# Kernel tuning notes

Measured on AMD Instinct MI355X. Metric: run time of the kernel, lower is better.

The kernel has to match this reference:

```python
import jax, jax.numpy as jnp
import numpy as np

N, E, C, NB, NE, G = 20000, 320000, 64, 8, 4, 16
L2 = 9          # (max_ell+1)^2 with max_ell=2
RMAX = 5.0
HID = 16        # nonlinear readout hidden width


def setup_inputs():
    key = jax.random.key(0)
    ks = jax.random.split(key, 16)
    positions = jax.random.uniform(ks[0], (N, 3), dtype=jnp.float32) * 3.0
    elems = jax.random.randint(ks[1], (N,), 0, NE)
    node_attrs = jax.nn.one_hot(elems, NE, dtype=jnp.float32)
    edge_index = jax.random.randint(ks[2], (2, E), 0, N)
    batch = jnp.sort(jax.random.randint(ks[3], (N,), 0, G))
    shifts = jnp.zeros((E, 3), jnp.float32)
    atomic_energies = jnp.array([-1.0, -2.0, -3.0, -4.0], jnp.float32)
    sc = lambda k, shp, fan: jax.random.normal(k, shp, jnp.float32) / np.sqrt(fan).astype(np.float32)
    W_embed = sc(ks[4], (NE, C), NE)
    W_up = sc(ks[5], (2, C, C), C)
    W1 = sc(ks[6], (2, NB, 64), NB)
    W2 = sc(ks[7], (2, 64, C), 64)
    W_out = sc(ks[8], (2, C, C), C)
    W_skip = sc(ks[9], (2, NE, C), NE)
    w_read0 = sc(ks[10], (C,), C)
    W_r1 = sc(ks[11], (C, HID), C)
    w_r2 = sc(ks[12], (HID,), HID)
    return dict(positions=positions, node_attrs=node_attrs, shifts=shifts,
                atomic_energies=atomic_energies, W_embed=W_embed, W_up=W_up,
                W1=W1, W2=W2, W_out=W_out, W_skip=W_skip, w_read0=w_read0,
                W_r1=W_r1, w_r2=w_r2, edge_index=edge_index, batch=batch)


def _sph_harm_l2(u):
    # component-normalized real spherical harmonics up to l=2 on unit vectors
    x, y, z = u[:, 0], u[:, 1], u[:, 2]
    s3, s5, s15 = jnp.sqrt(3.0), jnp.sqrt(5.0), jnp.sqrt(15.0)
    return jnp.stack([jnp.ones_like(x),
                      s3 * x, s3 * y, s3 * z,
                      s15 * x * y, s15 * y * z, 0.5 * s5 * (3.0 * z * z - 1.0),
                      s15 * x * z, 0.5 * s15 * (x * x - y * y)], axis=-1)


def _radial(r):
    # Bessel radial basis with polynomial cutoff (p=6)
    n = jnp.arange(1, NB + 1, dtype=jnp.float32)
    rb = jnp.sqrt(2.0 / RMAX) * jnp.sin(n * jnp.pi * r[:, None] / RMAX) / r[:, None]
    u = r / RMAX
    fc = 1.0 - 28.0 * u**6 + 48.0 * u**7 - 21.0 * u**8
    fc = jnp.where(u < 1.0, fc, 0.0)
    return rb * fc[:, None]


def _energy_contributions(positions, node_attrs, shifts, atomic_energies,
                          W_embed, W_up, W1, W2, W_out, W_skip,
                          w_read0, W_r1, w_r2, edge_index, batch):
    snd, rcv = edge_index[0], edge_index[1]
    vec = positions[snd] - positions[rcv] + shifts                  # [E,3]
    r = jnp.sqrt(jnp.sum(vec * vec, axis=-1) + 1e-12)               # [E]
    Y = _sph_harm_l2(vec / r[:, None])                              # [E,L2]
    ef = _radial(r)                                                 # [E,NB]
    # E0: per-element reference energies, summed per graph
    e0 = jax.ops.segment_sum(node_attrs @ atomic_energies, batch, num_segments=G)
    h0 = node_attrs @ W_embed                                       # [N,C] scalar feats
    h = jnp.zeros((positions.shape[0], L2, C), h0.dtype).at[:, 0, :].set(h0)
    readouts = [lambda s: s @ w_read0,
                lambda s: jax.nn.silu(s @ W_r1) @ w_r2]             # linear / nonlinear
    energies = [e0]
    for i in range(2):
        hu = jnp.einsum('nlc,cd->nld', h, W_up[i])                  # channel mix
        R = jax.nn.silu(ef @ W1[i]) @ W2[i]                         # radial MLP [E,C]
        s = jnp.einsum('elc,el->ec', hu[snd], Y)                    # equivariant contraction
        m = Y[:, :, None] * (R * s)[:, None, :]                     # [E,L2,C] messages
        agg = jax.ops.segment_sum(m, rcv, num_segments=positions.shape[0])
        h = jnp.einsum('nlc,cd->nld', agg, W_out[i])
        h = h.at[:, 0, :].add(node_attrs @ W_skip[i])               # scalar skip connection
        node_en = readouts[i](h[:, 0, :])                           # [N]
        energies.append(jax.ops.segment_sum(node_en, batch, num_segments=G))
    return jnp.stack(energies, axis=-1)                             # [G, num_interactions+1]


def reference(positions, node_attrs, shifts, atomic_energies, W_embed, W_up,
              W1, W2, W_out, W_skip, w_read0, W_r1, w_r2, edge_index, batch):
    contributions = _energy_contributions(positions, node_attrs, shifts,
        atomic_energies, W_embed, W_up, W1, W2, W_out, W_skip,
        w_read0, W_r1, w_r2, edge_index, batch)
    total_energy = jnp.sum(contributions, axis=-1)                  # [G]
    forces = -jax.grad(lambda p: jnp.sum(_energy_contributions(p, node_attrs,
        shifts, atomic_energies, W_embed, W_up, W1, W2, W_out, W_skip,
        w_read0, W_r1, w_r2, edge_index, batch)))(positions)        # [N,3]
    return total_energy, contributions, forces
```

## Files before the change

kernel.cpp:

```cpp
#include <hip/hip_runtime.h>
#include <cmath>

constexpr int N_  = 20000;
constexpr int E_  = 320000;
constexpr int NE_ = 4;
constexpr int G_  = 16;
constexpr int CAP = 96;
constexpr int TAB = 4096;
constexpr float RMAXF = 5.0f;
constexpr float PI_F  = 3.14159265358979323846f;
constexpr float S3  = 1.7320508075688772f;
constexpr float S5  = 2.2360679774997896f;
constexpr float S15 = 3.8729833462074170f;
constexpr float KC_ = 0.6324555320336759f;

typedef unsigned short u16;
typedef unsigned int   u32;
typedef _Float16 f16;
typedef _Float16 f16x2 __attribute__((ext_vector_type(2)));

#define DEV static __device__ __forceinline__

__device__ float g_fallback[110000000];

DEV float sigmoidf_(float x){ return 1.0f/(1.0f+__expf(-x)); }

DEV float b2f(u16 u){ return __uint_as_float(((u32)u)<<16); }
DEV u16  f2b(float f){
  u32 x = __float_as_uint(f);
  return (u16)((x + 0x7FFFu + ((x>>16)&1u)) >> 16);
}
DEV u16  f2h(float f){ union{f16 h; u16 u;} v; v.h=(f16)f; return v.u; }
DEV float h2f(u16 u){ union{u16 u2; f16 h;} v; v.u2=u; return (float)v.h; }

DEV f16x2 u2h(u32 x){ union{u32 u; f16x2 h;} v; v.u=x; return v.h; }
DEV u32 h2u(f16x2 h){ union{u32 u; f16x2 h;} v; v.h=h; return v.u; }
DEV u32 pkh(float a, float b){ f16x2 h; h.x=(f16)a; h.y=(f16)b; return h2u(h); }

DEV void ld4(const float* __restrict__ p, float* d){
  float4 a = ((const float4*)p)[0];
  d[0]=a.x; d[1]=a.y; d[2]=a.z; d[3]=a.w;
}
DEV void st8h(u16* p, const float* d){
  uint4 v;
  v.x = pkh(d[0],d[1]); v.y = pkh(d[2],d[3]);
  v.z = pkh(d[4],d[5]); v.w = pkh(d[6],d[7]);
  *(uint4*)p = v;
}
DEV void ldY(const u16* __restrict__ p, float* Yb){
  ushort4 a = *(const ushort4*)p;
  ushort4 b = *(const ushort4*)(p+4);
  Yb[0]=h2f(a.x); Yb[1]=h2f(a.y); Yb[2]=h2f(a.z); Yb[3]=h2f(a.w);
  Yb[4]=h2f(b.x); Yb[5]=h2f(b.y); Yb[6]=h2f(b.z); Yb[7]=h2f(b.w);
}

DEV float tlerp(const u16* __restrict__ tab, int i0, float f, int idx){
  return h2f(tab[i0*256+idx])*(1.0f-f) + h2f(tab[(i0+1)*256+idx])*f;
}

__global__ void k_cnt(const int* __restrict__ ei, int* __restrict__ cntR){
  int e = blockIdx.x*256 + threadIdx.x;
  atomicAdd(&cntR[ei[E_+e]], 1);
}

__global__ void k_scan(const int* __restrict__ cntR, int* __restrict__ offR){
  __shared__ int part[256];
  int t = threadIdx.x;
  constexpr int CH = (N_+255)/256;
  int base = t*CH;
  int s=0;
  for (int i=0;i<CH;++i){ int idx=base+i; if(idx<N_) s+=cntR[idx]; }
  part[t]=s; __syncthreads();
  for (int d=1; d<256; d<<=1){
    int v = (t>=d)? part[t-d] : 0;
    __syncthreads();
    part[t]+=v;
    __syncthreads();
  }
  int run = (t==0)?0:part[t-1];
  for (int i=0;i<CH;++i){ int idx=base+i; if(idx<N_){ offR[idx]=run; run+=cntR[idx]; } }
  if (t==255) offR[N_]=run;
}

__global__ void k_perm(const int* __restrict__ ei, const int* __restrict__ offR,
                       int* __restrict__ cntR2, int* __restrict__ cntS,
                       int* __restrict__ pe, int* __restrict__ pSnd, int* __restrict__ pRcv,
                       int* __restrict__ listS){
  int e = blockIdx.x*256 + threadIdx.x;
  int s = ei[e], r = ei[E_+e];
  int p = offR[r] + atomicAdd(&cntR2[r], 1);
  pe[p] = e; pSnd[p] = s; pRcv[p] = r;
  int q = atomicAdd(&cntS[s], 1); if (q < CAP) listS[s*CAP+q] = p;
}

__global__ void k_pre(const float* __restrict__ Wout0, const float* __restrict__ Wup1,
                      const float* __restrict__ Wskip0, const float* __restrict__ wread0,
                      const float* __restrict__ Wemb, const float* __restrict__ Wup0,
                      const float* __restrict__ Wr1, const float* __restrict__ Wout1,
                      float* __restrict__ WA, float* __restrict__ sa,
                      float* __restrict__ va, float* __restrict__ sv,
                      float* __restrict__ WembUp, float* __restrict__ CC){
  int t = threadIdx.x;
  for (int idx=t; idx<4096; idx+=256){
    int c = idx>>6, d = idx&63;
    float acc=0.f;
    for (int m=0;m<64;++m) acc += Wout0[c*64+m]*Wup1[m*64+d];
    WA[idx]=acc;
  }
  {
    int k = t>>6, d = t&63;
    float acc=0.f;
    for (int m=0;m<64;++m) acc += Wskip0[k*64+m]*Wup1[m*64+d];
    sa[t]=acc;
    float acc2=0.f;
    for (int j=0;j<64;++j) acc2 += Wemb[k*64+j]*Wup0[j*64+d];
    WembUp[t]=acc2;
  }
  for (int idx=t; idx<1024; idx+=256){
    int j = idx>>6, c = idx&63;
    float acc=0.f;
    for (int k=0;k<64;++k) acc += Wr1[k*16+j]*Wout1[c*64+k];
    CC[idx]=acc;
  }
  if (t<64){
    float acc=0.f;
    for (int d=0;d<64;++d) acc += Wout0[t*64+d]*wread0[d];
    va[t]=acc;
  }
  if (t<4){
    float acc=0.f;
    for (int d=0;d<64;++d) acc += Wskip0[t*64+d]*wread0[d];
    sv[t]=acc;
  }
}

__global__ __launch_bounds__(256, 2)
void k_rtab(const float* __restrict__ W1g, const float* __restrict__ W2g,
            u16* __restrict__ tab){
  __shared__ float sW1[1024];
  __shared__ u32   sW2h[4096];
  __shared__ u32   sAh[32*36];
  int t = threadIdx.x;
  for (int i=t;i<1024;i+=256) sW1[i]=W1g[i];
  for (int i=t;i<4096;i+=256){
    int L = i>>11, rem = i&2047, kp = rem>>6, c = rem&63;
    sW2h[i] = pkh(W2g[L*4096 + (2*kp)*64 + c], W2g[L*4096 + (2*kp+1)*64 + c]);
  }
  __syncthreads();
  int wid=t>>6, lane=t&63, q=lane>>3, j=lane&7, c0=j*8;
  int slot = wid*8 + q;
  int knot = blockIdx.x*32 + slot;
  bool valid = (knot <= TAB);
  float rad = fmaxf((float)knot * (RMAXF/(float)TAB), 1e-6f);
  float inv = 1.0f/rad;
  float tt = rad*(1.0f/RMAXF);
  float fc = 0.0f, dfc = 0.0f;
  if (tt < 1.0f){
    float t2=tt*tt, t4=t2*t2, t5=t4*tt, t6=t5*tt, t7=t6*tt, t8=t7*tt;
    fc  = 1.0f - 28.0f*t6 + 48.0f*t7 - 21.0f*t8;
    dfc = (-168.0f*t5 + 336.0f*t6 - 168.0f*t7)*(1.0f/RMAXF);
  }
  float th = rad*(PI_F/RMAXF);
  float s1 = __sinf(th), c1 = __cosf(th);
  float base = KC_*inv*fc;
  float efv[8], gfv[8];
  {
    float sb = s1, cb = c1;
    #pragma unroll
    for (int b=0;b<8;++b){
      efv[b] = base*sb;
      float wb_ = (float)(b+1)*(PI_F/RMAXF);
      float rb  = KC_*sb*inv;
      float drb = KC_*(wb_*cb - sb*inv)*inv;
      gfv[b] = drb*fc + rb*dfc;
      float sn = sb*c1 + cb*s1;
      cb = cb*c1 - sb*s1;
      sb = sn;
    }
  }
  u32* myAh = sAh + slot*36;
  for (int L=0; L<2; ++L){
    const float* w1 = sW1 + L*512;
    const u32*  w2h = sW2h + L*2048;
    float zz[8]={0,0,0,0,0,0,0,0};
    float wgv[8]={0,0,0,0,0,0,0,0};
    #pragma unroll 4
    for (int b=0;b<8;++b){
      float efb = efv[b], gfb = gfv[b];
      const float4* w=(const float4*)(w1 + b*64 + c0);
      float4 wa=w[0], wb=w[1];
      zz[0]+=efb*wa.x; zz[1]+=efb*wa.y; zz[2]+=efb*wa.z; zz[3]+=efb*wa.w;
      zz[4]+=efb*wb.x; zz[5]+=efb*wb.y; zz[6]+=efb*wb.z; zz[7]+=efb*wb.w;
      wgv[0]+=gfb*wa.x; wgv[1]+=gfb*wa.y; wgv[2]+=gfb*wa.z; wgv[3]+=gfb*wa.w;
      wgv[4]+=gfb*wb.x; wgv[5]+=gfb*wb.y; wgv[6]+=gfb*wb.z; wgv[7]+=gfb*wb.w;
    }
    float a[8], dv[8];
    #pragma unroll
    for (int i=0;i<8;++i){
      float sg = sigmoidf_(zz[i]);
      a[i]  = zz[i]*sg;
      float sp = sg*(1.0f + zz[i]*(1.0f - sg));
      dv[i] = wgv[i]*sp;
    }
    {
      uint4 av;
      av.x = pkh(a[0],a[1]); av.y = pkh(a[2],a[3]);
      av.z = pkh(a[4],a[5]); av.w = pkh(a[6],a[7]);
      *(uint4*)(myAh + 4*j) = av;
    }
    {
      float r0=0.f,r1=0.f,r2=0.f,r3=0.f,r4=0.f,r5=0.f,r6=0.f,r7=0.f;
      #pragma unroll 2
      for (int kp4=0; kp4<8; ++kp4){
        uint4 dq = *(const uint4*)(myAh + 4*kp4);
        #pragma unroll
        for (int i=0;i<4;++i){
          u32 du = (i==0)?dq.x:(i==1)?dq.y:(i==2)?dq.z:dq.w;
          f16x2 dh = u2h(du);
          const u32* wrow = w2h + (4*kp4+i)*64 + c0;
          uint4 w0 = *(const uint4*)(wrow);
          uint4 w1v = *(const uint4*)(wrow+4);
          r0 = __builtin_amdgcn_fdot2(dh, u2h(w0.x),  r0, false);
          r1 = __builtin_amdgcn_fdot2(dh, u2h(w0.y),  r1, false);
          r2 = __builtin_amdgcn_fdot2(dh, u2h(w0.z),  r2, false);
          r3 = __builtin_amdgcn_fdot2(dh, u2h(w0.w),  r3, false);
          r4 = __builtin_amdgcn_fdot2(dh, u2h(w1v.x), r4, false);
          r5 = __builtin_amdgcn_fdot2(dh, u2h(w1v.y), r5, false);
          r6 = __builtin_amdgcn_fdot2(dh, u2h(w1v.z), r6, false);
          r7 = __builtin_amdgcn_fdot2(dh, u2h(w1v.w), r7, false);
        }
      }
      float racc[8] = {r0,r1,r2,r3,r4,r5,r6,r7};
      if (valid) st8h(tab + (size_t)knot*256 + L*64 + c0, racc);
    }
    {
      uint4 av;
      av.x = pkh(dv[0],dv[1]); av.y = pkh(dv[2],dv[3]);
      av.z = pkh(dv[4],dv[5]); av.w = pkh(dv[6],dv[7]);
      *(uint4*)(myAh + 4*j) = av;
    }
    {
      float r0=0.f,r1=0.f,r2=0.f,r3=0.f,r4=0.f,r5=0.f,r6=0.f,r7=0.f;
      #pragma unroll 2
      for (int kp4=0; kp4<8; ++kp4){
        uint4 dq = *(const uint4*)(myAh + 4*kp4);
        #pragma unroll
        for (int i=0;i<4;++i){
          u32 du = (i==0)?dq.x:(i==1)?dq.y:(i==2)?dq.z:dq.w;
          f16x2 dh = u2h(du);
          const u32* wrow = w2h + (4*kp4+i)*64 + c0;
          uint4 w0 = *(const uint4*)(wrow);
          uint4 w1v = *(const uint4*)(wrow+4);
          r0 = __builtin_amdgcn_fdot2(dh, u2h(w0.x),  r0, false);
          r1 = __builtin_amdgcn_fdot2(dh, u2h(w0.y),  r1, false);
          r2 = __builtin_amdgcn_fdot2(dh, u2h(w0.z),  r2, false);
          r3 = __builtin_amdgcn_fdot2(dh, u2h(w0.w),  r3, false);
          r4 = __builtin_amdgcn_fdot2(dh, u2h(w1v.x), r4, false);
          r5 = __builtin_amdgcn_fdot2(dh, u2h(w1v.y), r5, false);
          r6 = __builtin_amdgcn_fdot2(dh, u2h(w1v.z), r6, false);
          r7 = __builtin_amdgcn_fdot2(dh, u2h(w1v.w), r7, false);
        }
      }
      float qacc[8] = {r0,r1,r2,r3,r4,r5,r6,r7};
      if (valid) st8h(tab + (size_t)knot*256 + 128 + L*64 + c0, qacc);
    }
  }
}

__global__ void k_fwd_edge(const float* __restrict__ pos, const float* __restrict__ shifts,
                const int* __restrict__ pe, const int* __restrict__ pSnd,
                const int* __restrict__ pRcv,
                u16* __restrict__ Y, float* __restrict__ u3,
                float* __restrict__ irr, float* __restrict__ xi){
  int e = blockIdx.x*256 + threadIdx.x;
  int eo  = pe[e];
  int snd = pSnd[e], rcv = pRcv[e];
  float vx = pos[snd*3+0]-pos[rcv*3+0]+shifts[(size_t)eo*3+0];
  float vy = pos[snd*3+1]-pos[rcv*3+1]+shifts[(size_t)eo*3+1];
  float vz = pos[snd*3+2]-pos[rcv*3+2]+shifts[(size_t)eo*3+2];
  float ss = vx*vx+vy*vy+vz*vz + 1e-12f;
  float rad = sqrtf(ss);
  float inv = 1.0f/rad;
  float x = vx*inv, y = vy*inv, z = vz*inv;
  irr[e]=inv;
  xi[e] = rad * ((float)TAB/RMAXF);
  u3[(size_t)e*3+0]=x; u3[(size_t)e*3+1]=y; u3[(size_t)e*3+2]=z;
  float Yf[8];
  Yf[0]=S3*x; Yf[1]=S3*y; Yf[2]=S3*z;
  Yf[3]=S15*x*y; Yf[4]=S15*y*z;
  Yf[5]=0.5f*S5*(3.0f*z*z-1.0f);
  Yf[6]=S15*x*z;
  Yf[7]=0.5f*S15*(x*x-y*y);
  st8h(Y + (size_t)e*8, Yf);
}

__global__ void k_agg0(const int* __restrict__ offR, const int* __restrict__ pSnd,
                       const float* __restrict__ attrs, const float* __restrict__ WembUp,
                       const u16* __restrict__ tab, const float* __restrict__ xi,
                       const u16* __restrict__ Y,
                       u16* __restrict__ agg0){
  int t = threadIdx.x; int n = blockIdx.x*4 + (t>>6); int c = t&63;
  float we0 = WembUp[0*64+c], we1 = WembUp[1*64+c], we2 = WembUp[2*64+c], we3 = WembUp[3*64+c];
  float acc[9] = {0,0,0,0,0,0,0,0,0};
  int p0 = offR[n], p1 = offR[n+1];
  for (int p=p0;p<p1;++p){
    int s = pSnd[p];
    float xiv = xi[p];
    float r0v = 0.f;
    if (xiv < (float)TAB){
      int i0 = (int)xiv; float f = xiv - (float)i0;
      r0v = tlerp(tab, i0, f, c);
    }
    float4 av = *(const float4*)(attrs + (size_t)s*4);
    float hu0c = av.x*we0 + av.y*we1 + av.z*we2 + av.w*we3;
    float v = r0v*hu0c;
    float Yb[8];
    ldY(Y + (size_t)p*8, Yb);
    acc[0] += v;
    #pragma unroll
    for (int l=1;l<9;++l) acc[l] += Yb[l-1]*v;
  }
  #pragma unroll
  for (int l=0;l<9;++l) agg0[((size_t)n*9+l)*64+c] = f2h(acc[l]);
}

__global__ void k_s1(const int* __restrict__ cntS, const int* __restrict__ listS,
                     const u16* __restrict__ hu1, const u16* __restrict__ Y,
                     u16* __restrict__ s1){
  int t = threadIdx.x; int n = blockIdx.x*4 + (t>>6); int c = t&63;
  float hu[9];
  #pragma unroll
  for (int l=0;l<9;++l) hu[l] = b2f(hu1[((size_t)n*9+l)*64+c]);
  int deg = min(cntS[n], CAP);
  #pragma unroll 2
  for (int j=0;j<deg;++j){
    int p = listS[n*CAP+j];
    float Yb[8];
    ldY(Y + (size_t)p*8, Yb);
    float acc = hu[0];
    #pragma unroll
    for (int l=1;l<9;++l) acc += hu[l]*Yb[l-1];
    s1[(size_t)p*64+c] = f2h(acc);
  }
}

__global__ void k_agg1(const int* __restrict__ offR,
                       const u16* __restrict__ tab, const float* __restrict__ xi,
                       const u16* __restrict__ s1,
                       float* __restrict__ agg1){
  int t = threadIdx.x; int n = blockIdx.x*4 + (t>>6); int c = t&63;
  float acc = 0.f;
  int p0 = offR[n], p1 = offR[n+1];
  for (int p=p0;p<p1;++p){
    float xiv = xi[p];
    float r1v = 0.f;
    if (xiv < (float)TAB){
      int i0 = (int)xiv; float f = xiv - (float)i0;
      r1v = tlerp(tab, i0, f, 64 + c);
    }
    acc += r1v*h2f(s1[(size_t)p*64+c]);
  }
  agg1[(size_t)n*64+c] = acc;
}

__global__ void k_dhu1(const int* __restrict__ cntS, const int* __restrict__ listS,
                       const int* __restrict__ pRcv,
                       const u16* __restrict__ tab, const float* __restrict__ xi,
                       const float* __restrict__ ga1, const u16* __restrict__ Y,
                       u16* __restrict__ dhu1){
  int t = threadIdx.x; int n = blockIdx.x*4 + (t>>6); int c = t&63;
  float acc[9] = {0,0,0,0,0,0,0,0,0};
  int deg = min(cntS[n], CAP);
  #pragma unroll 2
  for (int j=0;j<deg;++j){
    int p = listS[n*CAP+j];
    int r = pRcv[p];
    float xiv = xi[p];
    float r1v = 0.f;
    if (xiv < (float)TAB){
      int i0 = (int)xiv; float f = xiv - (float)i0;
      r1v = tlerp(tab, i0, f, 64 + c);
    }
    float ds = r1v*ga1[(size_t)r*64+c];
    float Yb[8];
    ldY(Y + (size_t)p*8, Yb);
    acc[0] += ds;
    #pragma unroll
    for (int l=1;l<9;++l) acc[l] += Yb[l-1]*ds;
  }
  #pragma unroll
  for (int l=0;l<9;++l) dhu1[((size_t)n*9+l)*64+c] = f2h(acc[l]);
}

template<bool TRANS, bool OUTB, bool IN16>
__global__ __launch_bounds__(256, 2)
void k_mm64(const void* __restrict__ in, const float* __restrict__ W,
            void* __restrict__ out, int rows, int lper,
            const float* __restrict__ attrs, const float* __restrict__ Wsk,
            const float* __restrict__ bias){
  __shared__ float sWT[64*68];
  __shared__ float sRow[4*68];
  int t = threadIdx.x;
  for (int i=t;i<4096;i+=256){
    int k=i&63, c=i>>6;
    sWT[c*68+k] = TRANS ? W[c*64+k] : W[k*64+c];
  }
  __syncthreads();
  int wid = t>>6, c = t&63;
  float wcol[64];
  {
    const float4* wp = (const float4*)(sWT + c*68);
    #pragma unroll
    for (int kk=0;kk<16;++kk){
      float4 w4 = wp[kk];
      wcol[4*kk+0]=w4.x; wcol[4*kk+1]=w4.y; wcol[4*kk+2]=w4.z; wcol[4*kk+3]=w4.w;
    }
  }
  float* myRow = sRow + wid*68;
  for (int it=0; it<8; ++it){
    int row = (blockIdx.x*8+it)*4 + wid;
    if (IN16) myRow[c] = h2f(((const u16*)in)[(size_t)row*64+c]);
    else      myRow[c] = ((const float*)in)[(size_t)row*64+c];
    float acc = 0.f;
    #pragma unroll
    for (int kk=0;kk<16;++kk){
      float4 r4 = ((const float4*)myRow)[kk];
      acc += r4.x*wcol[4*kk+0] + r4.y*wcol[4*kk+1] + r4.z*wcol[4*kk+2] + r4.w*wcol[4*kk+3];
    }
    if (lper==1 || (row % 9)==0){
      int n = (lper==1) ? row : (row/9);
      if (attrs){
        #pragma unroll
        for (int k=0;k<NE_;++k) acc += attrs[n*NE_+k]*Wsk[k*64+c];
      }
      if (bias) acc += bias[c];
    }
    if (OUTB) ((u16*)out)[(size_t)row*64+c] = f2b(acc);
    else      ((float*)out)[(size_t)row*64+c] = acc;
  }
}

__global__ void k_read0(const u16* __restrict__ agg0, const float* __restrict__ va,
                        const float* __restrict__ sv, const float* __restrict__ attrs,
                        const float* __restrict__ ae,
                        const int* __restrict__ batch, float* __restrict__ out){
  __shared__ float bins0[G_];
  __shared__ float bins1[G_];
  int t = threadIdx.x;
  if (t < G_){ bins0[t] = 0.f; bins1[t] = 0.f; }
  __syncthreads();
  int lane = t & 63, wid = t >> 6;
  int grp = lane >> 3, j = lane & 7;
  int n = blockIdx.x*32 + wid*8 + grp;
  const u16* hp = agg0 + (size_t)n*576 + j*8;
  float h[8];
  ldY(hp, h);
  const float* wp = va + j*8;
  float4 w0v = ((const float4*)wp)[0], w4v = ((const float4*)wp)[1];
  float v = h[0]*w0v.x + h[1]*w0v.y + h[2]*w0v.z + h[3]*w0v.w
          + h[4]*w4v.x + h[5]*w4v.y + h[6]*w4v.z + h[7]*w4v.w;
  v += __shfl_xor(v,1,64); v += __shfl_xor(v,2,64); v += __shfl_xor(v,4,64);
  if (j==0){
    float4 av = *(const float4*)(attrs + (size_t)n*4);
    v += av.x*sv[0] + av.y*sv[1] + av.z*sv[2] + av.w*sv[3];
    float e0v = av.x*ae[0] + av.y*ae[1] + av.z*ae[2] + av.w*ae[3];
    int b = batch[n];
    atomicAdd(&bins1[b], v);
    atomicAdd(&bins0[b], e0v);
  }
  __syncthreads();
  if (t < G_){
    float b0 = bins0[t], b1 = bins1[t];
    if (b0 != 0.f || b1 != 0.f){
      atomicAdd(&out[t], b0 + b1);
      if (b0 != 0.f) atomicAdd(&out[G_ + t*3 + 0], b0);
      if (b1 != 0.f) atomicAdd(&out[G_ + t*3 + 1], b1);
    }
  }
}

__global__ void k_read1(const float* __restrict__ h2, const float* __restrict__ Wr1,
                        const float* __restrict__ wr2, const int* __restrict__ batch,
                        const float* __restrict__ CC,
                        float* __restrict__ ga1, float* __restrict__ out){
  __shared__ float sW[64*16];
  __shared__ float sCC[16*64];
  __shared__ float sSp[256];
  __shared__ float sA[256];
  __shared__ float bins[G_];
  int t = threadIdx.x;
  for (int i=t;i<1024;i+=256){ sW[i]=Wr1[i]; sCC[i]=CC[i]; }
  if (t < G_) bins[t] = 0.f;
  __syncthreads();
  int nn = t>>4; int j = t&15;
  int n = blockIdx.x*16 + nn;
  float z = 0.f;
  #pragma unroll 16
  for (int c=0;c<64;++c) z += h2[(size_t)n*64+c]*sW[c*16+j];
  float sg = sigmoidf_(z);
  float a  = z*sg;
  float sp = sg*(1.0f + z*(1.0f - sg));
  float w2v = wr2[j];
  sSp[t] = sp*w2v;
  sA[t]  = a*w2v;
  __syncthreads();
  {
    int cb = j*4;
    float g0=0.f,g1=0.f,g2=0.f,g3=0.f;
    const float* sp_ = sSp + nn*16;
    #pragma unroll
    for (int jp=0;jp<16;++jp){
      float s = sp_[jp];
      const float* cc = sCC + jp*64 + cb;
      g0 += s*cc[0]; g1 += s*cc[1]; g2 += s*cc[2]; g3 += s*cc[3];
    }
    *(float4*)(ga1 + (size_t)n*64 + cb) = make_float4(g0,g1,g2,g3);
  }
  if (j==0){
    float s = 0.f;
    #pragma unroll
    for (int k=0;k<16;++k) s += sA[nn*16+k];
    atomicAdd(&bins[batch[n]], s);
  }
  __syncthreads();
  if (t < G_){
    float b = bins[t];
    if (b != 0.f){
      atomicAdd(&out[t], b);
      atomicAdd(&out[G_ + t*3 + 2], b);
    }
  }
}

__global__ __launch_bounds__(256, 4)
void k_bedge_all(const int* __restrict__ pSnd, const int* __restrict__ pRcv,
             const u16* __restrict__ Y,
             const float* __restrict__ u3, const float* __restrict__ irr,
             const u16* __restrict__ tab, const float* __restrict__ xi,
             const float* __restrict__ ga1, const u16* __restrict__ ga0,
             const float* __restrict__ attrs, const float* __restrict__ WembUp,
             const u16* __restrict__ hu1,
             float* __restrict__ gF){
  int t = threadIdx.x;
  int wid=t>>6, lane=t&63, q=lane>>4, j=lane&15, c0=j*4;
  int slot = wid*4+q;
  int e = blockIdx.x*16 + slot;
  int snd = pSnd[e], rcv = pRcv[e];
  float wembr[4][4];
  #pragma unroll
  for (int k=0;k<4;++k){
    float4 wr = *(const float4*)(WembUp + k*64 + c0);
    wembr[k][0]=wr.x; wembr[k][1]=wr.y; wembr[k][2]=wr.z; wembr[k][3]=wr.w;
  }
  float Yl[9];
  Yl[0]=1.0f;
  ldY(Y + (size_t)e*8, Yl+1);
  ushort4 huv1[9];
  #pragma unroll
  for (int l=0;l<9;++l) huv1[l] = *(const ushort4*)(hu1 + ((size_t)snd*9 + l)*64 + c0);
  ushort4 gv0[9];
  #pragma unroll
  for (int l=0;l<9;++l) gv0[l] = *(const ushort4*)(ga0 + ((size_t)rcv*9 + l)*64 + c0);
  float T1[4];  ld4(ga1 + (size_t)rcv*64 + c0, T1);
  float4 av = *(const float4*)(attrs + (size_t)snd*4);
  float hu0v[4];
  #pragma unroll
  for (int i=0;i<4;++i)
    hu0v[i] = av.x*wembr[0][i] + av.y*wembr[1][i] + av.z*wembr[2][i] + av.w*wembr[3][i];
  float xiv = xi[e];
  float R0v[4], R1v[4], q0v[4], q1v[4];
  if (xiv < (float)TAB){
    int i0 = (int)xiv; float f = xiv - (float)i0, g = 1.0f - f;
    const u16* ra = tab + (size_t)i0*256;
    const u16* rb = ra + 256;
    ushort4 a, b;
    a = *(const ushort4*)(ra + c0);        b = *(const ushort4*)(rb + c0);
    R0v[0]=h2f(a.x)*g+h2f(b.x)*f; R0v[1]=h2f(a.y)*g+h2f(b.y)*f;
    R0v[2]=h2f(a.z)*g+h2f(b.z)*f; R0v[3]=h2f(a.w)*g+h2f(b.w)*f;
    a = *(const ushort4*)(ra + 64 + c0);   b = *(const ushort4*)(rb + 64 + c0);
    R1v[0]=h2f(a.x)*g+h2f(b.x)*f; R1v[1]=h2f(a.y)*g+h2f(b.y)*f;
    R1v[2]=h2f(a.z)*g+h2f(b.z)*f; R1v[3]=h2f(a.w)*g+h2f(b.w)*f;
    a = *(const ushort4*)(ra + 128 + c0);  b = *(const ushort4*)(rb + 128 + c0);
    q0v[0]=h2f(a.x)*g+h2f(b.x)*f; q0v[1]=h2f(a.y)*g+h2f(b.y)*f;
    q0v[2]=h2f(a.z)*g+h2f(b.z)*f; q0v[3]=h2f(a.w)*g+h2f(b.w)*f;
    a = *(const ushort4*)(ra + 192 + c0);  b = *(const ushort4*)(rb + 192 + c0);
    q1v[0]=h2f(a.x)*g+h2f(b.x)*f; q1v[1]=h2f(a.y)*g+h2f(b.y)*f;
    q1v[2]=h2f(a.z)*g+h2f(b.z)*f; q1v[3]=h2f(a.w)*g+h2f(b.w)*f;
  } else {
    #pragma unroll
    for (int i=0;i<4;++i){ R0v[i]=0.f; R1v[i]=0.f; q0v[i]=0.f; q1v[i]=0.f; }
  }
  float dyp[9];
  float dR1[4];
  {
    float ds1[4], sA[4];
    #pragma unroll
    for (int i=0;i<4;++i){ ds1[i]=R1v[i]*T1[i]; sA[i]=0.f; }
    #pragma unroll
    for (int l=0;l<9;++l){
      float h0v=b2f(huv1[l].x), h1v=b2f(huv1[l].y), h2v=b2f(huv1[l].z), h3v=b2f(huv1[l].w);
      float Ylv = Yl[l];
      sA[0]+=h0v*Ylv; sA[1]+=h1v*Ylv; sA[2]+=h2v*Ylv; sA[3]+=h3v*Ylv;
      dyp[l] = ds1[0]*h0v + ds1[1]*h1v + ds1[2]*h2v + ds1[3]*h3v;
    }
    #pragma unroll
    for (int i=0;i<4;++i) dR1[i]=sA[i]*T1[i];
  }
  float dR0[4];
  {
    float P[4], T0[4];
    #pragma unroll
    for (int i=0;i<4;++i){ P[i]=R0v[i]*hu0v[i]; T0[i]=0.f; }
    #pragma unroll
    for (int l=0;l<9;++l){
      float g0=b2f(gv0[l].x), g1=b2f(gv0[l].y), g2=b2f(gv0[l].z), g3=b2f(gv0[l].w);
      float Ylv = Yl[l];
      T0[0]+=g0*Ylv; T0[1]+=g1*Ylv; T0[2]+=g2*Ylv; T0[3]+=g3*Ylv;
      dyp[l] += g0*P[0] + g1*P[1] + g2*P[2] + g3*P[3];
    }
    #pragma unroll
    for (int i=0;i<4;++i) dR0[i]=hu0v[i]*T0[i];
  }
  float dy[9];
  #pragma unroll
  for (int l=1;l<9;++l){
    float v=dyp[l];
    v += __shfl_xor(v,1,64); v += __shfl_xor(v,2,64);
    v += __shfl_xor(v,4,64); v += __shfl_xor(v,8,64);
    dy[l]=v;
  }
  float dr = q1v[0]*dR1[0]+q1v[1]*dR1[1]+q1v[2]*dR1[2]+q1v[3]*dR1[3]
           + q0v[0]*dR0[0]+q0v[1]*dR0[1]+q0v[2]*dR0[2]+q0v[3]*dR0[3];
  dr += __shfl_xor(dr,1,64); dr += __shfl_xor(dr,2,64);
  dr += __shfl_xor(dr,4,64); dr += __shfl_xor(dr,8,64);
  float x = u3[(size_t)e*3+0], y = u3[(size_t)e*3+1], zz = u3[(size_t)e*3+2];
  float invr = irr[e];
  float dux = S3*dy[1] + S15*(y*dy[4] + zz*dy[7] + x*dy[8]);
  float duy = S3*dy[2] + S15*(x*dy[4] + zz*dy[5] - y*dy[8]);
  float duz = S3*dy[3] + S15*(y*dy[5] + x*dy[7]) + 3.0f*S5*zz*dy[6];
  float udot = x*dux + y*duy + zz*duz;
  float gx = dr*x + invr*(dux - x*udot);
  float gy = dr*y + invr*(duy - y*udot);
  float gz = dr*zz + invr*(duz - zz*udot);
  if (j==0){
    float* gp2 = gF + (size_t)e*3;
    gp2[0]=gx; gp2[1]=gy; gp2[2]=gz;
  }
}

__global__ void k_fsum(const int* __restrict__ offR, const int* __restrict__ cntS,
                       const int* __restrict__ listS,
                       const float* __restrict__ gF, float* __restrict__ F){
  int t = threadIdx.x;
  int lane = t & 63, wid = t >> 6;
  int sub = lane >> 3, j = lane & 7;
  int n = blockIdx.x*32 + wid*8 + sub;
  float fx=0.f, fy=0.f, fz=0.f;
  int p0 = offR[n], p1 = offR[n+1];
  for (int p=p0+j; p<p1; p+=8){
    fx += gF[(size_t)p*3+0]; fy += gF[(size_t)p*3+1]; fz += gF[(size_t)p*3+2];
  }
  int dSn = min(cntS[n], CAP);
  for (int k=j;k<dSn;k+=8){
    int p = listS[n*CAP+k];
    fx -= gF[(size_t)p*3+0]; fy -= gF[(size_t)p*3+1]; fz -= gF[(size_t)p*3+2];
  }
  fx += __shfl_xor(fx,1,64); fy += __shfl_xor(fy,1,64); fz += __shfl_xor(fz,1,64);
  fx += __shfl_xor(fx,2,64); fy += __shfl_xor(fy,2,64); fz += __shfl_xor(fz,2,64);
  fx += __shfl_xor(fx,4,64); fy += __shfl_xor(fy,4,64); fz += __shfl_xor(fz,4,64);
  if (j==0){
    F[n*3+0]=fx; F[n*3+1]=fy; F[n*3+2]=fz;
  }
}

extern "C" void kernel_launch(void* const* d_in, const int* in_sizes, int n_in,
                              void* d_out, int out_size, void* d_ws, size_t ws_size,
                              hipStream_t stream){
  (void)in_sizes; (void)n_in;
  const float* pos    = (const float*)d_in[0];
  const float* attrs  = (const float*)d_in[1];
  const float* shifts = (const float*)d_in[2];
  const float* ae     = (const float*)d_in[3];
  const float* Wemb   = (const float*)d_in[4];
  const float* Wup    = (const float*)d_in[5];
  const float* W1     = (const float*)d_in[6];
  const float* W2     = (const float*)d_in[7];
  const float* Wout   = (const float*)d_in[8];
  const float* Wskip  = (const float*)d_in[9];
  const float* wread0 = (const float*)d_in[10];
  const float* Wr1    = (const float*)d_in[11];
  const float* wr2    = (const float*)d_in[12];
  const int*   ei     = (const int*)d_in[13];
  const int*   batch  = (const int*)d_in[14];
  float* out = (float*)d_out;

  const size_t NEED = 430000000;
  char* base;
  if (ws_size >= NEED){
    base = (char*)d_ws;
  } else {
    void* p = nullptr;
    hipGetSymbolAddress(&p, HIP_SYMBOL(g_fallback));
    base = (char*)p;
  }
  size_t off = 0;
  auto alloc = [&](size_t bytes)->char*{
    char* p = base + off;
    off += ((bytes + 255)/256)*256;
    return p;
  };
  u16*   Y    = (u16*)  alloc((size_t)E_*8*2);
  float* u3   = (float*)alloc((size_t)E_*3*4);
  float* irr  = (float*)alloc((size_t)E_*4);
  float* xi   = (float*)alloc((size_t)E_*4);
  u16*   s1b  = (u16*)  alloc((size_t)E_*64*2);
  float* gF   = (float*)alloc((size_t)E_*3*4);
  u16*   tab  = (u16*)  alloc((size_t)(TAB+1)*256*2);
  u16*   hu1  = (u16*)  alloc((size_t)N_*9*64*2);
  u16*   agg0 = (u16*)  alloc((size_t)N_*9*64*2);
  float* agg1 = (float*)alloc((size_t)N_*64*4);
  float* h2   = (float*)alloc((size_t)N_*64*4);
  float* ga1  = (float*)alloc((size_t)N_*64*4);
  u16*   ga0  = (u16*)  alloc((size_t)N_*9*64*2);
  float* WembUp = (float*)alloc(256*4);
  float* WA   = (float*)alloc(4096*4);
  float* sa   = (float*)alloc(256*4);
  float* va   = (float*)alloc(64*4);
  float* sv   = (float*)alloc(4*4);
  float* CC   = (float*)alloc(1024*4);
  int* cnts  = (int*)alloc((size_t)3*N_*4);
  int* offR  = (int*)alloc((size_t)(N_+1)*4);
  int* pe    = (int*)alloc((size_t)E_*4);
  int* pSnd  = (int*)alloc((size_t)E_*4);
  int* pRcv  = (int*)alloc((size_t)E_*4);
  int* listS = (int*)alloc((size_t)N_*CAP*4);
  int* cntR = cnts;  int* cntS = cnts + N_;  int* cntR2 = cnts + 2*N_;
  u16* dhu1 = agg0;
  float* F = out + G_ + G_*3;

  hipMemsetAsync(d_out, 0, (size_t)out_size*sizeof(float), stream);
  hipMemsetAsync(cnts, 0, (size_t)3*N_*sizeof(int), stream);

  k_cnt     <<<E_/256, 256, 0, stream>>>(ei, cntR);
  k_scan    <<<1, 256, 0, stream>>>(cntR, offR);
  k_perm    <<<E_/256, 256, 0, stream>>>(ei, offR, cntR2, cntS, pe, pSnd, pRcv, listS);

  k_rtab    <<<(TAB+1+31)/32, 256, 0, stream>>>(W1, W2, tab);
  k_fwd_edge<<<E_/256, 256, 0, stream>>>(pos, shifts, pe, pSnd, pRcv, Y, u3, irr, xi);
  k_pre     <<<1, 256, 0, stream>>>(Wout, Wup + 4096, Wskip, wread0, Wemb, Wup, Wr1, Wout + 4096, WA, sa, va, sv, WembUp, CC);
  k_agg0    <<<N_/4, 256, 0, stream>>>(offR, pSnd, attrs, WembUp, tab, xi, Y, agg0);
  k_mm64<false,true,true><<<N_*9/32, 256, 0, stream>>>(agg0, WA, hu1, N_*9, 9, attrs, sa, nullptr);
  k_read0   <<<N_/32, 256, 0, stream>>>(agg0, va, sv, attrs, ae, batch, out);
  k_s1      <<<N_/4, 256, 0, stream>>>(cntS, listS, hu1, Y, s1b);
  k_agg1    <<<N_/4, 256, 0, stream>>>(offR, tab, xi, s1b, agg1);
  k_mm64<false,false,false><<<N_/32, 256, 0, stream>>>(agg1, Wout + 4096, h2, N_, 1, attrs, Wskip + 256, nullptr);
  k_read1   <<<N_/16, 256, 0, stream>>>(h2, Wr1, wr2, batch, CC, ga1, out);

  k_dhu1    <<<N_/4, 256, 0, stream>>>(cntS, listS, pRcv, tab, xi, ga1, Y, dhu1);
  k_mm64<true,true,true><<<N_*9/32, 256, 0, stream>>>(dhu1, WA, ga0, N_*9, 9, nullptr, nullptr, va);
  k_bedge_all<<<E_/16, 256, 0, stream>>>(pSnd, pRcv, Y, u3, irr, tab, xi, ga1, ga0, attrs, WembUp, hu1, gF);
  k_fsum    <<<N_/32, 256, 0, stream>>>(offR, cntS, listS, gF, F);
}
```

Before: 727.6 us.

## Split per-node edge loops across two wavefronts and defer loads in backward edge kernel

```diff
diff --git a/kernel.cpp b/kernel.cpp
--- a/kernel.cpp
+++ b/kernel.cpp
@@ -299,11 +299,14 @@
                        const u16* __restrict__ tab, const float* __restrict__ xi,
                        const u16* __restrict__ Y,
                        u16* __restrict__ agg0){
-  int t = threadIdx.x; int n = blockIdx.x*4 + (t>>6); int c = t&63;
+  __shared__ float red[2][9][64];
+  int t = threadIdx.x; int wid = t>>6; int c = t&63;
+  int nl = wid>>1, half = wid&1;
+  int n = blockIdx.x*2 + nl;
   float we0 = WembUp[0*64+c], we1 = WembUp[1*64+c], we2 = WembUp[2*64+c], we3 = WembUp[3*64+c];
   float acc[9] = {0,0,0,0,0,0,0,0,0};
   int p0 = offR[n], p1 = offR[n+1];
-  for (int p=p0;p<p1;++p){
+  for (int p=p0+half; p<p1; p+=2){
     int s = pSnd[p];
     float xiv = xi[p];
     float r0v = 0.f;
@@ -320,20 +323,28 @@
     #pragma unroll
     for (int l=1;l<9;++l) acc[l] += Yb[l-1]*v;
   }
-  #pragma unroll
-  for (int l=0;l<9;++l) agg0[((size_t)n*9+l)*64+c] = f2h(acc[l]);
+  if (half==1){
+    #pragma unroll
+    for (int l=0;l<9;++l) red[nl][l][c] = acc[l];
+  }
+  __syncthreads();
+  if (half==0){
+    #pragma unroll
+    for (int l=0;l<9;++l) agg0[((size_t)n*9+l)*64+c] = f2h(acc[l] + red[nl][l][c]);
+  }
 }
 
 __global__ void k_s1(const int* __restrict__ cntS, const int* __restrict__ listS,
                      const u16* __restrict__ hu1, const u16* __restrict__ Y,
                      u16* __restrict__ s1){
-  int t = threadIdx.x; int n = blockIdx.x*4 + (t>>6); int c = t&63;
+  int t = threadIdx.x; int wid = t>>6; int c = t&63;
+  int nl = wid>>1, half = wid&1;
+  int n = blockIdx.x*2 + nl;
   float hu[9];
   #pragma unroll
   for (int l=0;l<9;++l) hu[l] = b2f(hu1[((size_t)n*9+l)*64+c]);
   int deg = min(cntS[n], CAP);
-  #pragma unroll 2
-  for (int j=0;j<deg;++j){
+  for (int j=half;j<deg;j+=2){
     int p = listS[n*CAP+j];
     float Yb[8];
     ldY(Y + (size_t)p*8, Yb);
@@ -348,10 +359,13 @@
                        const u16* __restrict__ tab, const float* __restrict__ xi,
                        const u16* __restrict__ s1,
                        float* __restrict__ agg1){
-  int t = threadIdx.x; int n = blockIdx.x*4 + (t>>6); int c = t&63;
+  __shared__ float red[2][64];
+  int t = threadIdx.x; int wid = t>>6; int c = t&63;
+  int nl = wid>>1, half = wid&1;
+  int n = blockIdx.x*2 + nl;
   float acc = 0.f;
   int p0 = offR[n], p1 = offR[n+1];
-  for (int p=p0;p<p1;++p){
+  for (int p=p0+half; p<p1; p+=2){
     float xiv = xi[p];
     float r1v = 0.f;
     if (xiv < (float)TAB){
@@ -360,7 +374,9 @@
     }
     acc += r1v*h2f(s1[(size_t)p*64+c]);
   }
-  agg1[(size_t)n*64+c] = acc;
+  if (half==1) red[nl][c] = acc;
+  __syncthreads();
+  if (half==0) agg1[(size_t)n*64+c] = acc + red[nl][c];
 }
 
 __global__ void k_dhu1(const int* __restrict__ cntS, const int* __restrict__ listS,
@@ -368,11 +384,13 @@
                        const u16* __restrict__ tab, const float* __restrict__ xi,
                        const float* __restrict__ ga1, const u16* __restrict__ Y,
                        u16* __restrict__ dhu1){
-  int t = threadIdx.x; int n = blockIdx.x*4 + (t>>6); int c = t&63;
+  __shared__ float red[2][9][64];
+  int t = threadIdx.x; int wid = t>>6; int c = t&63;
+  int nl = wid>>1, half = wid&1;
+  int n = blockIdx.x*2 + nl;
   float acc[9] = {0,0,0,0,0,0,0,0,0};
   int deg = min(cntS[n], CAP);
-  #pragma unroll 2
-  for (int j=0;j<deg;++j){
+  for (int j=half;j<deg;j+=2){
     int p = listS[n*CAP+j];
     int r = pRcv[p];
     float xiv = xi[p];
@@ -388,8 +406,15 @@
     #pragma unroll
     for (int l=1;l<9;++l) acc[l] += Yb[l-1]*ds;
   }
-  #pragma unroll
-  for (int l=0;l<9;++l) dhu1[((size_t)n*9+l)*64+c] = f2h(acc[l]);
+  if (half==1){
+    #pragma unroll
+    for (int l=0;l<9;++l) red[nl][l][c] = acc[l];
+  }
+  __syncthreads();
+  if (half==0){
+    #pragma unroll
+    for (int l=0;l<9;++l) dhu1[((size_t)n*9+l)*64+c] = f2h(acc[l] + red[nl][l][c]);
+  }
 }
 
 template<bool TRANS, bool OUTB, bool IN16>
@@ -546,27 +571,14 @@
   int slot = wid*4+q;
   int e = blockIdx.x*16 + slot;
   int snd = pSnd[e], rcv = pRcv[e];
-  float wembr[4][4];
-  #pragma unroll
-  for (int k=0;k<4;++k){
-    float4 wr = *(const float4*)(WembUp + k*64 + c0);
-    wembr[k][0]=wr.x; wembr[k][1]=wr.y; wembr[k][2]=wr.z; wembr[k][3]=wr.w;
-  }
   float Yl[9];
   Yl[0]=1.0f;
   ldY(Y + (size_t)e*8, Yl+1);
   ushort4 huv1[9];
   #pragma unroll
   for (int l=0;l<9;++l) huv1[l] = *(const ushort4*)(hu1 + ((size_t)snd*9 + l)*64 + c0);
-  ushort4 gv0[9];
-  #pragma unroll
-  for (int l=0;l<9;++l) gv0[l] = *(const ushort4*)(ga0 + ((size_t)rcv*9 + l)*64 + c0);
   float T1[4];  ld4(ga1 + (size_t)rcv*64 + c0, T1);
   float4 av = *(const float4*)(attrs + (size_t)snd*4);
-  float hu0v[4];
-  #pragma unroll
-  for (int i=0;i<4;++i)
-    hu0v[i] = av.x*wembr[0][i] + av.y*wembr[1][i] + av.z*wembr[2][i] + av.w*wembr[3][i];
   float xiv = xi[e];
   float R0v[4], R1v[4], q0v[4], q1v[4];
   if (xiv < (float)TAB){
@@ -606,8 +618,16 @@
     #pragma unroll
     for (int i=0;i<4;++i) dR1[i]=sA[i]*T1[i];
   }
+  float hu0v[4];
+  #pragma unroll
+  for (int i=0;i<4;++i)
+    hu0v[i] = av.x*WembUp[0*64+c0+i] + av.y*WembUp[1*64+c0+i]
+            + av.z*WembUp[2*64+c0+i] + av.w*WembUp[3*64+c0+i];
   float dR0[4];
   {
+    ushort4 gv0[9];
+    #pragma unroll
+    for (int l=0;l<9;++l) gv0[l] = *(const ushort4*)(ga0 + ((size_t)rcv*9 + l)*64 + c0);
     float P[4], T0[4];
     #pragma unroll
     for (int i=0;i<4;++i){ P[i]=R0v[i]*hu0v[i]; T0[i]=0.f; }
@@ -748,15 +768,15 @@
   k_rtab    <<<(TAB+1+31)/32, 256, 0, stream>>>(W1, W2, tab);
   k_fwd_edge<<<E_/256, 256, 0, stream>>>(pos, shifts, pe, pSnd, pRcv, Y, u3, irr, xi);
   k_pre     <<<1, 256, 0, stream>>>(Wout, Wup + 4096, Wskip, wread0, Wemb, Wup, Wr1, Wout + 4096, WA, sa, va, sv, WembUp, CC);
-  k_agg0    <<<N_/4, 256, 0, stream>>>(offR, pSnd, attrs, WembUp, tab, xi, Y, agg0);
+  k_agg0    <<<N_/2, 256, 0, stream>>>(offR, pSnd, attrs, WembUp, tab, xi, Y, agg0);
   k_mm64<false,true,true><<<N_*9/32, 256, 0, stream>>>(agg0, WA, hu1, N_*9, 9, attrs, sa, nullptr);
   k_read0   <<<N_/32, 256, 0, stream>>>(agg0, va, sv, attrs, ae, batch, out);
-  k_s1      <<<N_/4, 256, 0, stream>>>(cntS, listS, hu1, Y, s1b);
-  k_agg1    <<<N_/4, 256, 0, stream>>>(offR, tab, xi, s1b, agg1);
+  k_s1      <<<N_/2, 256, 0, stream>>>(cntS, listS, hu1, Y, s1b);
+  k_agg1    <<<N_/2, 256, 0, stream>>>(offR, tab, xi, s1b, agg1);
   k_mm64<false,false,false><<<N_/32, 256, 0, stream>>>(agg1, Wout + 4096, h2, N_, 1, attrs, Wskip + 256, nullptr);
   k_read1   <<<N_/16, 256, 0, stream>>>(h2, Wr1, wr2, batch, CC, ga1, out);
 
-  k_dhu1    <<<N_/4, 256, 0, stream>>>(cntS, listS, pRcv, tab, xi, ga1, Y, dhu1);
+  k_dhu1    <<<N_/2, 256, 0, stream>>>(cntS, listS, pRcv, tab, xi, ga1, Y, dhu1);
   k_mm64<true,true,true><<<N_*9/32, 256, 0, stream>>>(dhu1, WA, ga0, N_*9, 9, nullptr, nullptr, va);
   k_bedge_all<<<E_/16, 256, 0, stream>>>(pSnd, pRcv, Y, u3, irr, tab, xi, ga1, ga0, attrs, WembUp, hu1, gF);
   k_fsum    <<<N_/32, 256, 0, stream>>>(offR, cntS, listS, gF, F);
```

Measured after the change: 731.4 us. No clear change (+0.5%).

## Fuse node matmuls with readout kernels and trim edge-backward register pressure

Applied to the files above, without the earlier changes.

```diff
diff --git a/kernel.cpp b/kernel.cpp
--- a/kernel.cpp
+++ b/kernel.cpp
@@ -440,33 +440,64 @@
   }
 }
 
-__global__ void k_read0(const u16* __restrict__ agg0, const float* __restrict__ va,
-                        const float* __restrict__ sv, const float* __restrict__ attrs,
-                        const float* __restrict__ ae,
-                        const int* __restrict__ batch, float* __restrict__ out){
+__global__ __launch_bounds__(256, 2)
+void k_mm64_read0(const u16* __restrict__ in, const float* __restrict__ W,
+                  u16* __restrict__ outB,
+                  const float* __restrict__ attrs, const float* __restrict__ Wsk,
+                  const float* __restrict__ va, const float* __restrict__ sv,
+                  const float* __restrict__ ae, const int* __restrict__ batch,
+                  float* __restrict__ out){
+  __shared__ float sWT[64*68];
+  __shared__ float sRow[4*68];
   __shared__ float bins0[G_];
   __shared__ float bins1[G_];
   int t = threadIdx.x;
-  if (t < G_){ bins0[t] = 0.f; bins1[t] = 0.f; }
+  if (t < G_){ bins0[t]=0.f; bins1[t]=0.f; }
+  for (int i=t;i<4096;i+=256){
+    int k=i&63, c=i>>6;
+    sWT[c*68+k] = W[k*64+c];
+  }
   __syncthreads();
-  int lane = t & 63, wid = t >> 6;
-  int grp = lane >> 3, j = lane & 7;
-  int n = blockIdx.x*32 + wid*8 + grp;
-  const u16* hp = agg0 + (size_t)n*576 + j*8;
-  float h[8];
-  ldY(hp, h);
-  const float* wp = va + j*8;
-  float4 w0v = ((const float4*)wp)[0], w4v = ((const float4*)wp)[1];
-  float v = h[0]*w0v.x + h[1]*w0v.y + h[2]*w0v.z + h[3]*w0v.w
-          + h[4]*w4v.x + h[5]*w4v.y + h[6]*w4v.z + h[7]*w4v.w;
-  v += __shfl_xor(v,1,64); v += __shfl_xor(v,2,64); v += __shfl_xor(v,4,64);
-  if (j==0){
-    float4 av = *(const float4*)(attrs + (size_t)n*4);
-    v += av.x*sv[0] + av.y*sv[1] + av.z*sv[2] + av.w*sv[3];
-    float e0v = av.x*ae[0] + av.y*ae[1] + av.z*ae[2] + av.w*ae[3];
-    int b = batch[n];
-    atomicAdd(&bins1[b], v);
-    atomicAdd(&bins0[b], e0v);
+  int wid = t>>6, c = t&63;
+  float vac = va[c];
+  float wcol[64];
+  {
+    const float4* wp = (const float4*)(sWT + c*68);
+    #pragma unroll
+    for (int kk=0;kk<16;++kk){
+      float4 w4 = wp[kk];
+      wcol[4*kk+0]=w4.x; wcol[4*kk+1]=w4.y; wcol[4*kk+2]=w4.z; wcol[4*kk+3]=w4.w;
+    }
+  }
+  float* myRow = sRow + wid*68;
+  for (int it=0; it<8; ++it){
+    int row = (blockIdx.x*8+it)*4 + wid;
+    float rv = h2f(in[(size_t)row*64+c]);
+    myRow[c] = rv;
+    float acc = 0.f;
+    #pragma unroll
+    for (int kk=0;kk<16;++kk){
+      float4 r4 = ((const float4*)myRow)[kk];
+      acc += r4.x*wcol[4*kk+0] + r4.y*wcol[4*kk+1] + r4.z*wcol[4*kk+2] + r4.w*wcol[4*kk+3];
+    }
+    if ((row % 9)==0){
+      int n = row/9;
+      #pragma unroll
+      for (int k=0;k<NE_;++k) acc += attrs[n*NE_+k]*Wsk[k*64+c];
+      float v = rv*vac;
+      v += __shfl_xor(v,1,64);  v += __shfl_xor(v,2,64);
+      v += __shfl_xor(v,4,64);  v += __shfl_xor(v,8,64);
+      v += __shfl_xor(v,16,64); v += __shfl_xor(v,32,64);
+      if (c==0){
+        float4 av = *(const float4*)(attrs + (size_t)n*4);
+        v += av.x*sv[0] + av.y*sv[1] + av.z*sv[2] + av.w*sv[3];
+        float e0v = av.x*ae[0] + av.y*ae[1] + av.z*ae[2] + av.w*ae[3];
+        int b = batch[n];
+        atomicAdd(&bins1[b], v);
+        atomicAdd(&bins0[b], e0v);
+      }
+    }
+    outB[(size_t)row*64+c] = f2b(acc);
   }
   __syncthreads();
   if (t < G_){
@@ -479,50 +510,77 @@
   }
 }
 
-__global__ void k_read1(const float* __restrict__ h2, const float* __restrict__ Wr1,
-                        const float* __restrict__ wr2, const int* __restrict__ batch,
-                        const float* __restrict__ CC,
-                        float* __restrict__ ga1, float* __restrict__ out){
+__global__ __launch_bounds__(256, 2)
+void k_mm64_read1(const float* __restrict__ in, const float* __restrict__ W,
+                  const float* __restrict__ attrs, const float* __restrict__ Wsk,
+                  const float* __restrict__ Wr1, const float* __restrict__ wr2,
+                  const float* __restrict__ CC, const int* __restrict__ batch,
+                  float* __restrict__ ga1, float* __restrict__ out){
+  __shared__ float sWT[64*68];
+  __shared__ float sRow[4*68];
   __shared__ float sW[64*16];
   __shared__ float sCC[16*64];
-  __shared__ float sSp[256];
-  __shared__ float sA[256];
+  __shared__ float sH[4][64];
+  __shared__ float sSp[4][16];
+  __shared__ float sA[4][16];
   __shared__ float bins[G_];
   int t = threadIdx.x;
+  if (t < G_) bins[t]=0.f;
+  for (int i=t;i<4096;i+=256){
+    int k=i&63, c=i>>6;
+    sWT[c*68+k] = W[k*64+c];
+  }
   for (int i=t;i<1024;i+=256){ sW[i]=Wr1[i]; sCC[i]=CC[i]; }
-  if (t < G_) bins[t] = 0.f;
   __syncthreads();
-  int nn = t>>4; int j = t&15;
-  int n = blockIdx.x*16 + nn;
-  float z = 0.f;
-  #pragma unroll 16
-  for (int c=0;c<64;++c) z += h2[(size_t)n*64+c]*sW[c*16+j];
-  float sg = sigmoidf_(z);
-  float a  = z*sg;
-  float sp = sg*(1.0f + z*(1.0f - sg));
-  float w2v = wr2[j];
-  sSp[t] = sp*w2v;
-  sA[t]  = a*w2v;
-  __syncthreads();
+  int wid = t>>6, c = t&63;
+  float wcol[64];
   {
-    int cb = j*4;
-    float g0=0.f,g1=0.f,g2=0.f,g3=0.f;
-    const float* sp_ = sSp + nn*16;
-    #pragma unroll
-    for (int jp=0;jp<16;++jp){
-      float s = sp_[jp];
-      const float* cc = sCC + jp*64 + cb;
-      g0 += s*cc[0]; g1 += s*cc[1]; g2 += s*cc[2]; g3 += s*cc[3];
-    }
-    *(float4*)(ga1 + (size_t)n*64 + cb) = make_float4(g0,g1,g2,g3);
-  }
-  if (j==0){
-    float s = 0.f;
-    #pragma unroll
-    for (int k=0;k<16;++k) s += sA[nn*16+k];
-    atomicAdd(&bins[batch[n]], s);
-  }
-  __syncthreads();
+    const float4* wp = (const float4*)(sWT + c*68);
+    #pragma unroll
+    for (int kk=0;kk<16;++kk){
+      float4 w4 = wp[kk];
+      wcol[4*kk+0]=w4.x; wcol[4*kk+1]=w4.y; wcol[4*kk+2]=w4.z; wcol[4*kk+3]=w4.w;
+    }
+  }
+  float* myRow = sRow + wid*68;
+  for (int it=0; it<8; ++it){
+    int n = (blockIdx.x*8+it)*4 + wid;
+    myRow[c] = in[(size_t)n*64+c];
+    float acc = 0.f;
+    #pragma unroll
+    for (int kk=0;kk<16;++kk){
+      float4 r4 = ((const float4*)myRow)[kk];
+      acc += r4.x*wcol[4*kk+0] + r4.y*wcol[4*kk+1] + r4.z*wcol[4*kk+2] + r4.w*wcol[4*kk+3];
+    }
+    #pragma unroll
+    for (int k=0;k<NE_;++k) acc += attrs[n*NE_+k]*Wsk[k*64+c];
+    sH[wid][c] = acc;
+    __syncthreads();
+    if (c < 16){
+      float z = 0.f;
+      const float* hr = sH[wid];
+      #pragma unroll 16
+      for (int k=0;k<64;++k) z += hr[k]*sW[k*16+c];
+      float sg = sigmoidf_(z);
+      float w2v = wr2[c];
+      sSp[wid][c] = sg*(1.0f + z*(1.0f - sg))*w2v;
+      sA[wid][c]  = z*sg*w2v;
+    }
+    __syncthreads();
+    {
+      float g = 0.f;
+      #pragma unroll
+      for (int jp=0;jp<16;++jp) g += sSp[wid][jp]*sCC[jp*64+c];
+      ga1[(size_t)n*64+c] = g;
+    }
+    if (c==0){
+      float s = 0.f;
+      #pragma unroll
+      for (int k=0;k<16;++k) s += sA[wid][k];
+      atomicAdd(&bins[batch[n]], s);
+    }
+    __syncthreads();
+  }
   if (t < G_){
     float b = bins[t];
     if (b != 0.f){
@@ -546,27 +604,14 @@
   int slot = wid*4+q;
   int e = blockIdx.x*16 + slot;
   int snd = pSnd[e], rcv = pRcv[e];
-  float wembr[4][4];
-  #pragma unroll
-  for (int k=0;k<4;++k){
-    float4 wr = *(const float4*)(WembUp + k*64 + c0);
-    wembr[k][0]=wr.x; wembr[k][1]=wr.y; wembr[k][2]=wr.z; wembr[k][3]=wr.w;
-  }
   float Yl[9];
   Yl[0]=1.0f;
   ldY(Y + (size_t)e*8, Yl+1);
   ushort4 huv1[9];
   #pragma unroll
   for (int l=0;l<9;++l) huv1[l] = *(const ushort4*)(hu1 + ((size_t)snd*9 + l)*64 + c0);
-  ushort4 gv0[9];
-  #pragma unroll
-  for (int l=0;l<9;++l) gv0[l] = *(const ushort4*)(ga0 + ((size_t)rcv*9 + l)*64 + c0);
   float T1[4];  ld4(ga1 + (size_t)rcv*64 + c0, T1);
   float4 av = *(const float4*)(attrs + (size_t)snd*4);
-  float hu0v[4];
-  #pragma unroll
-  for (int i=0;i<4;++i)
-    hu0v[i] = av.x*wembr[0][i] + av.y*wembr[1][i] + av.z*wembr[2][i] + av.w*wembr[3][i];
   float xiv = xi[e];
   float R0v[4], R1v[4], q0v[4], q1v[4];
   if (xiv < (float)TAB){
@@ -606,8 +651,16 @@
     #pragma unroll
     for (int i=0;i<4;++i) dR1[i]=sA[i]*T1[i];
   }
+  float hu0v[4];
+  #pragma unroll
+  for (int i=0;i<4;++i)
+    hu0v[i] = av.x*WembUp[0*64+c0+i] + av.y*WembUp[1*64+c0+i]
+            + av.z*WembUp[2*64+c0+i] + av.w*WembUp[3*64+c0+i];
   float dR0[4];
   {
+    ushort4 gv0[9];
+    #pragma unroll
+    for (int l=0;l<9;++l) gv0[l] = *(const ushort4*)(ga0 + ((size_t)rcv*9 + l)*64 + c0);
     float P[4], T0[4];
     #pragma unroll
     for (int i=0;i<4;++i){ P[i]=R0v[i]*hu0v[i]; T0[i]=0.f; }
@@ -719,7 +772,6 @@
   u16*   hu1  = (u16*)  alloc((size_t)N_*9*64*2);
   u16*   agg0 = (u16*)  alloc((size_t)N_*9*64*2);
   float* agg1 = (float*)alloc((size_t)N_*64*4);
-  float* h2   = (float*)alloc((size_t)N_*64*4);
   float* ga1  = (float*)alloc((size_t)N_*64*4);
   u16*   ga0  = (u16*)  alloc((size_t)N_*9*64*2);
   float* WembUp = (float*)alloc(256*4);
@@ -749,12 +801,10 @@
   k_fwd_edge<<<E_/256, 256, 0, stream>>>(pos, shifts, pe, pSnd, pRcv, Y, u3, irr, xi);
   k_pre     <<<1, 256, 0, stream>>>(Wout, Wup + 4096, Wskip, wread0, Wemb, Wup, Wr1, Wout + 4096, WA, sa, va, sv, WembUp, CC);
   k_agg0    <<<N_/4, 256, 0, stream>>>(offR, pSnd, attrs, WembUp, tab, xi, Y, agg0);
-  k_mm64<false,true,true><<<N_*9/32, 256, 0, stream>>>(agg0, WA, hu1, N_*9, 9, attrs, sa, nullptr);
-  k_read0   <<<N_/32, 256, 0, stream>>>(agg0, va, sv, attrs, ae, batch, out);
+  k_mm64_read0<<<N_*9/32, 256, 0, stream>>>(agg0, WA, hu1, attrs, sa, va, sv, ae, batch, out);
   k_s1      <<<N_/4, 256, 0, stream>>>(cntS, listS, hu1, Y, s1b);
   k_agg1    <<<N_/4, 256, 0, stream>>>(offR, tab, xi, s1b, agg1);
-  k_mm64<false,false,false><<<N_/32, 256, 0, stream>>>(agg1, Wout + 4096, h2, N_, 1, attrs, Wskip + 256, nullptr);
-  k_read1   <<<N_/16, 256, 0, stream>>>(h2, Wr1, wr2, batch, CC, ga1, out);
+  k_mm64_read1<<<N_/32, 256, 0, stream>>>(agg1, Wout + 4096, attrs, Wskip + 256, Wr1, wr2, CC, batch, ga1, out);
 
   k_dhu1    <<<N_/4, 256, 0, stream>>>(cntS, listS, pRcv, tab, xi, ga1, Y, dhu1);
   k_mm64<true,true,true><<<N_*9/32, 256, 0, stream>>>(dhu1, WA, ga0, N_*9, 9, nullptr, nullptr, va);
```

New measurement: 766.5 us. 5.3% more time.
